# Kernel tuning notes

Hardware: AMD Instinct MI355X
Metric: run time of the kernel (lower is better)

## Reference

```python
import jax, jax.numpy as jnp
import numpy as np

N_NODES = 100000
N_EDGES = 1600000
IN_FEAT = 64
OUT_FEAT = 64


def setup_inputs() -> dict:
    key = jax.random.key(0)
    k_feat, k_src, k_dst, k_tw, k_tb, k_pw, k_pb = jax.random.split(key, 7)
    bound = 1.0 / np.sqrt(IN_FEAT)
    return {
        "feat": jax.random.normal(k_feat, (N_NODES, IN_FEAT), dtype=jnp.float32),
        "src": jax.random.randint(k_src, (N_EDGES,), 0, N_NODES, dtype=jnp.int32),
        "dst": jax.random.randint(k_dst, (N_EDGES,), 0, N_NODES, dtype=jnp.int32),
        "theta_w": jax.random.uniform(k_tw, (OUT_FEAT, IN_FEAT), jnp.float32, -bound, bound),
        "theta_b": jax.random.uniform(k_tb, (OUT_FEAT,), jnp.float32, -bound, bound),
        "phi_w": jax.random.uniform(k_pw, (OUT_FEAT, IN_FEAT), jnp.float32, -bound, bound),
        "phi_b": jax.random.uniform(k_pb, (OUT_FEAT,), jnp.float32, -bound, bound),
    }


def reference(feat, src, dst, theta_w, theta_b, phi_w, phi_b):
    # Two dense projections: h_theta = theta(feat), h_phi = phi(feat)
    h_theta = feat @ theta_w.T + theta_b          # [N, out_feat]
    h_phi = feat @ phi_w.T + phi_b                # [N, out_feat]
    diff = h_phi - h_theta                        # dstdata['x']
    # u_add_v: per-edge message e = h_theta[src] + (h_phi - h_theta)[dst]
    e = h_theta[src] + diff[dst]                  # [E, out_feat]
    # fn.max('e', 'x'): segment max over destination nodes
    out = jax.ops.segment_max(e, dst, num_segments=N_NODES)  # [N, out_feat]
    # DGL fills zero-in-degree destinations with 0 (segment_max yields -inf)
    return jnp.where(jnp.isfinite(out), out, jnp.float32(0))
```

## Files before the change

kernel.cpp:

```cpp
#include <hip/hip_runtime.h>
#include <hip/hip_bf16.h>
#include <hip/hip_fp16.h>

#define F 64
#define BSH 7
#define NBMAX 1024
#define CHUNK 4096
#define EPT 8
#define BCAP 4096
#define WPAD 72

typedef __bf16 bf16x8 __attribute__((ext_vector_type(8)));
typedef float  f32x4  __attribute__((ext_vector_type(4)));
typedef unsigned int uint4v __attribute__((ext_vector_type(4)));

__device__ inline unsigned pkmax(unsigned a, unsigned b) {
    unsigned d;
    asm volatile("v_pk_max_f16 %0, %1, %2" : "=v"(d) : "v"(a), "v"(b));
    return d;
}
__device__ inline uint4v pkmax4(uint4v a, uint4v b) {
    uint4v r;
    r.x = pkmax(a.x, b.x); r.y = pkmax(a.y, b.y);
    r.z = pkmax(a.z, b.z); r.w = pkmax(a.w, b.w);
    return r;
}
__device__ inline float half_lo(unsigned u) {
    union { unsigned short s; _Float16 h; } c; c.s = (unsigned short)(u & 0xFFFF);
    return (float)c.h;
}
__device__ inline float half_hi(unsigned u) {
    union { unsigned short s; _Float16 h; } c; c.s = (unsigned short)(u >> 16);
    return (float)c.h;
}

union FusedSh {
    struct { __bf16 w2t[128 * WPAD]; float bias[128]; } p;
    struct { int cur[NBMAX]; int gb[NBMAX]; } b;
};

__global__ __launch_bounds__(512) void fused_proj_bin(
    const float* __restrict__ feat,
    const float* __restrict__ theta_w, const float* __restrict__ theta_b,
    const float* __restrict__ phi_w,  const float* __restrict__ phi_b,
    _Float16* __restrict__ h16, _Float16* __restrict__ d16,
    const int* __restrict__ src, const int* __restrict__ dst,
    int* __restrict__ bcnt, unsigned* __restrict__ packed,
    int n_nodes, int n_edges, int nb, int bin_blocks, int proj_blocks)
{
    __shared__ FusedSh sh;
    const int t = threadIdx.x;

    if (blockIdx.x < bin_blocks) {
        const int base = blockIdx.x * CHUNK;
        const int cnt = min(CHUNK, n_edges - base);

        for (int i = t; i < nb; i += 512) sh.b.cur[i] = 0;
        __syncthreads();

        unsigned w[EPT];
        int      bk[EPT];
        int      rk[EPT];
        const int k0 = t * EPT;

        if (k0 + EPT <= cnt) {
            #pragma unroll
            for (int j = 0; j < EPT; ++j) {
                int k = k0 + j;
                int s = src[base + k], d = dst[base + k];
                w[j]  = ((unsigned)(d & ((1 << BSH) - 1)) << 17) | (unsigned)s;
                int b = d >> BSH;
                bk[j] = b;
                rk[j] = atomicAdd(&sh.b.cur[b], 1);
            }
        } else {
            #pragma unroll
            for (int j = 0; j < EPT; ++j) {
                int k = k0 + j;
                bk[j] = -1;
                if (k < cnt) {
                    int s = src[base + k], d = dst[base + k];
                    w[j]  = ((unsigned)(d & ((1 << BSH) - 1)) << 17) | (unsigned)s;
                    int b = d >> BSH;
                    bk[j] = b;
                    rk[j] = atomicAdd(&sh.b.cur[b], 1);
                }
            }
        }
        __syncthreads();

        for (int i = t; i < nb; i += 512) {
            int c = sh.b.cur[i];
            sh.b.gb[i] = c ? atomicAdd(&bcnt[i], c) : 0;
        }
        __syncthreads();

        #pragma unroll
        for (int j = 0; j < EPT; ++j) {
            if (bk[j] >= 0) {
                int pos = sh.b.gb[bk[j]] + rk[j];
                if (pos < BCAP) packed[(size_t)bk[j] * BCAP + pos] = w[j];
            }
        }
    } else {
        const int pb = blockIdx.x - bin_blocks;

        for (int i = t; i < 128 * 64; i += 512) {
            int n = i >> 6, k = i & 63;
            float v = (n < 64) ? theta_w[n * 64 + k]
                               : phi_w[(n - 64) * 64 + k] - theta_w[(n - 64) * 64 + k];
            sh.p.w2t[n * WPAD + k] = (__bf16)v;
        }
        if (t < 128) {
            int n = t;
            sh.p.bias[n] = (n < 64) ? theta_b[n] : (phi_b[n - 64] - theta_b[n - 64]);
        }
        __syncthreads();

        const int lane = t & 63;
        const int wv   = t >> 6;
        const int m    = lane & 15;
        const int q    = lane >> 4;
        const int nchunks = (n_nodes + 127) >> 7;

        for (int ch = pb; ch < nchunks; ch += proj_blocks) {
            const int rowbase = ch * 128 + wv * 16;
            int arow = rowbase + m;
            int rs = arow < n_nodes ? arow : 0;

            bf16x8 a0, a1;
            {
                const float* p0 = feat + (size_t)rs * 64 + q * 8;
                #pragma unroll
                for (int j = 0; j < 8; ++j) a0[j] = (__bf16)p0[j];
                #pragma unroll
                for (int j = 0; j < 8; ++j) a1[j] = (__bf16)p0[32 + j];
            }

            f32x4 acc[8];
            #pragma unroll
            for (int c = 0; c < 8; ++c) acc[c] = (f32x4){0.f, 0.f, 0.f, 0.f};

            #pragma unroll
            for (int c = 0; c < 8; ++c) {
                const __bf16* wp = &sh.p.w2t[(c * 16 + m) * WPAD + q * 8];
                bf16x8 b0 = *(const bf16x8*)wp;
                bf16x8 b1 = *(const bf16x8*)(wp + 32);
                acc[c] = __builtin_amdgcn_mfma_f32_16x16x32_bf16(a0, b0, acc[c], 0, 0, 0);
                acc[c] = __builtin_amdgcn_mfma_f32_16x16x32_bf16(a1, b1, acc[c], 0, 0, 0);
            }

            #pragma unroll
            for (int c = 0; c < 8; ++c) {
                float bb = sh.p.bias[c * 16 + m];
                #pragma unroll
                for (int r = 0; r < 4; ++r) {
                    int orow = rowbase + q * 4 + r;
                    if (orow < n_nodes) {
                        float v = acc[c][r] + bb;
                        if (c < 4)
                            h16[(size_t)orow * F + c * 16 + m] = (_Float16)v;
                        else
                            d16[(size_t)orow * F + (c - 4) * 16 + m] = (_Float16)v;
                    }
                }
            }
        }
    }
}

__global__ __launch_bounds__(256) void fine_kernel(
    const unsigned* __restrict__ packed, const int* __restrict__ bcnt,
    int* __restrict__ row_beg, int* __restrict__ row_end,
    int* __restrict__ sorted_src, int n_nodes)
{
    __shared__ int fcnt[128];
    __shared__ int fbeg[128];
    __shared__ int fs[256];

    const int b = blockIdx.x, t = threadIdx.x;
    const int beg = b * BCAP;
    const int cnt = min(bcnt[b], BCAP);

    if (t < 128) fcnt[t] = 0;
    __syncthreads();

    unsigned w[16];
    int      rk[16];
    #pragma unroll
    for (int j = 0; j < 16; ++j) {
        int k = j * 256 + t;
        rk[j] = -1;
        if (k < cnt) {
            unsigned wrd = packed[beg + k];
            w[j]  = wrd;
            rk[j] = atomicAdd(&fcnt[wrd >> 17], 1);
        }
    }
    __syncthreads();

    int v = (t < 128) ? fcnt[t] : 0;
    fs[t] = v;
    __syncthreads();
    for (int off = 1; off < 128; off <<= 1) {
        int x = (t >= off) ? fs[t - off] : 0;
        __syncthreads();
        fs[t] += x;
        __syncthreads();
    }
    if (t < 128) {
        int exc = fs[t] - v;
        int node = (b << BSH) + t;
        if (node < n_nodes) {
            row_beg[node] = beg + exc;
            row_end[node] = beg + exc + v;
        }
        fbeg[t] = beg + exc;
    }
    __syncthreads();

    #pragma unroll
    for (int j = 0; j < 16; ++j) {
        if (rk[j] >= 0) {
            int node = w[j] >> 17;
            sorted_src[fbeg[node] + rk[j]] = (int)(w[j] & 0x1FFFFu);
        }
    }
}

__global__ __launch_bounds__(256) void reduce_kernel(
    const int* __restrict__ row_beg, const int* __restrict__ row_end,
    const int* __restrict__ sorted_src,
    const _Float16* __restrict__ h16, const _Float16* __restrict__ d16,
    float* __restrict__ out, int n_nodes)
{
    const int wid  = (blockIdx.x * blockDim.x + threadIdx.x) >> 6;
    const int lane = threadIdx.x & 63;
    const int g    = lane >> 3;
    const int f8   = lane & 7;

    const int node = wid * 8 + g;
    const int nc   = node < n_nodes ? node : n_nodes - 1;

    const int beg = row_beg[nc];
    const int end = row_end[nc];
    const int deg = end - beg;
    const int last = beg + (deg > 0 ? deg - 1 : 0);

    int mdeg = deg;
    mdeg = max(mdeg, __shfl_xor(mdeg, 8));
    mdeg = max(mdeg, __shfl_xor(mdeg, 16));
    mdeg = max(mdeg, __shfl_xor(mdeg, 32));

    const unsigned NEG = 0xFC00FC00u;
    uint4v A = (uint4v){NEG, NEG, NEG, NEG};
    uint4v B = (uint4v){NEG, NEG, NEG, NEG};
    uint4v C = (uint4v){NEG, NEG, NEG, NEG};
    uint4v D = (uint4v){NEG, NEG, NEG, NEG};

    for (int e = 0; e < mdeg; e += 4) {
        int p0 = beg + e;     p0 = p0 < last ? p0 : last;
        int p1 = beg + e + 1; p1 = p1 < last ? p1 : last;
        int p2 = beg + e + 2; p2 = p2 < last ? p2 : last;
        int p3 = beg + e + 3; p3 = p3 < last ? p3 : last;
        int i0 = sorted_src[p0];
        int i1 = sorted_src[p1];
        int i2 = sorted_src[p2];
        int i3 = sorted_src[p3];
        uint4v v0 = *(const uint4v*)(h16 + (size_t)i0 * F + f8 * 8);
        uint4v v1 = *(const uint4v*)(h16 + (size_t)i1 * F + f8 * 8);
        uint4v v2 = *(const uint4v*)(h16 + (size_t)i2 * F + f8 * 8);
        uint4v v3 = *(const uint4v*)(h16 + (size_t)i3 * F + f8 * 8);
        A = pkmax4(A, v0);
        B = pkmax4(B, v1);
        C = pkmax4(C, v2);
        D = pkmax4(D, v3);
    }

    A = pkmax4(A, B);
    C = pkmax4(C, D);
    A = pkmax4(A, C);

    if (node < n_nodes) {
        size_t o = (size_t)node * F + f8 * 8;
        f32x4 r0, r1;
        if (deg > 0) {
            uint4v dv = __builtin_nontemporal_load((const uint4v*)(d16 + o));
            r0[0] = half_lo(dv.x) + half_lo(A.x);
            r0[1] = half_hi(dv.x) + half_hi(A.x);
            r0[2] = half_lo(dv.y) + half_lo(A.y);
            r0[3] = half_hi(dv.y) + half_hi(A.y);
            r1[0] = half_lo(dv.z) + half_lo(A.z);
            r1[1] = half_hi(dv.z) + half_hi(A.z);
            r1[2] = half_lo(dv.w) + half_lo(A.w);
            r1[3] = half_hi(dv.w) + half_hi(A.w);
        } else {
            r0 = (f32x4){0.f, 0.f, 0.f, 0.f};
            r1 = (f32x4){0.f, 0.f, 0.f, 0.f};
        }
        __builtin_nontemporal_store(r0, (f32x4*)(out + o));
        __builtin_nontemporal_store(r1, (f32x4*)(out + o + 4));
    }
}

extern "C" void kernel_launch(void* const* d_in, const int* in_sizes, int n_in,
                              void* d_out, int out_size, void* d_ws, size_t ws_size,
                              hipStream_t stream) {
    const float* feat    = (const float*)d_in[0];
    const int*   src     = (const int*)d_in[1];
    const int*   dst     = (const int*)d_in[2];
    const float* theta_w = (const float*)d_in[3];
    const float* theta_b = (const float*)d_in[4];
    const float* phi_w   = (const float*)d_in[5];
    const float* phi_b   = (const float*)d_in[6];
    float* out = (float*)d_out;

    const int n_nodes = in_sizes[0] / F;
    const int n_edges = in_sizes[1];
    const int nb      = (n_nodes + (1 << BSH) - 1) >> BSH;

    _Float16* h16        = (_Float16*)d_ws;
    _Float16* d16        = h16 + (size_t)n_nodes * F;
    unsigned* packed     = (unsigned*)(d16 + (size_t)n_nodes * F);
    int*      sorted_src = (int*)(packed + (size_t)nb * BCAP);
    int*      row_beg    = sorted_src + (size_t)nb * BCAP;
    int*      row_end    = row_beg + n_nodes;
    int*      bcnt       = row_end + n_nodes;

    hipMemsetAsync(bcnt, 0, NBMAX * sizeof(int), stream);

    const int bin_blocks  = (n_edges + CHUNK - 1) / CHUNK;
    const int proj_blocks = 391;
    fused_proj_bin<<<bin_blocks + proj_blocks, 512, 0, stream>>>(
        feat, theta_w, theta_b, phi_w, phi_b, h16, d16,
        src, dst, bcnt, packed, n_nodes, n_edges, nb, bin_blocks, proj_blocks);

    fine_kernel<<<nb, 256, 0, stream>>>(packed, bcnt, row_beg, row_end,
                                        sorted_src, n_nodes);

    int waves   = (n_nodes + 7) / 8;
    int rblocks = (waves * 64 + 255) / 256;
    reduce_kernel<<<rblocks, 256, 0, stream>>>(row_beg, row_end, sorted_src,
                                               h16, d16, out, n_nodes);
}
```

Baseline: 158.5 us.

## Fuse fine sort and reduce into one bucket kernel using LDS atomic max

Replaces the per-bucket counting sort kernel and the CSR-based gather-reduce kernel with a single kernel per 128-node bucket. Each block gathers source rows and folds them into a 128x64 shared-memory table with atomicMax on order-preserving float keys, then adds the destination term and writes out. This drops the sorted_src/row_beg/row_end round trip and one launch, at the cost of eight LDS atomics per gathered 8-element chunk, possible contention, and 32 KB of shared memory per block, which may limit occupancy.

Measured after the change: 187.9 us. 18.6% more time.

```diff
diff --git a/kernel.cpp b/kernel.cpp
--- a/kernel.cpp
+++ b/kernel.cpp
@@ -13,18 +13,8 @@
 typedef __bf16 bf16x8 __attribute__((ext_vector_type(8)));
 typedef float  f32x4  __attribute__((ext_vector_type(4)));
 typedef unsigned int uint4v __attribute__((ext_vector_type(4)));
-
-__device__ inline unsigned pkmax(unsigned a, unsigned b) {
-    unsigned d;
-    asm volatile("v_pk_max_f16 %0, %1, %2" : "=v"(d) : "v"(a), "v"(b));
-    return d;
-}
-__device__ inline uint4v pkmax4(uint4v a, uint4v b) {
-    uint4v r;
-    r.x = pkmax(a.x, b.x); r.y = pkmax(a.y, b.y);
-    r.z = pkmax(a.z, b.z); r.w = pkmax(a.w, b.w);
-    return r;
-}
+typedef unsigned int uint2v __attribute__((ext_vector_type(2)));
+
 __device__ inline float half_lo(unsigned u) {
     union { unsigned short s; _Float16 h; } c; c.s = (unsigned short)(u & 0xFFFF);
     return (float)c.h;
@@ -32,6 +22,14 @@
 __device__ inline float half_hi(unsigned u) {
     union { unsigned short s; _Float16 h; } c; c.s = (unsigned short)(u >> 16);
     return (float)c.h;
+}
+__device__ inline unsigned f32key(float x) {
+    unsigned u = __float_as_uint(x);
+    return u ^ (unsigned)(((int)u >> 31) | 0x80000000);
+}
+__device__ inline float keyf32(unsigned k) {
+    unsigned u = k ^ (unsigned)(~((int)k >> 31) | 0x80000000);
+    return __uint_as_float(u);
 }
 
 union FusedSh {
@@ -169,137 +167,62 @@
     }
 }
 
-__global__ __launch_bounds__(256) void fine_kernel(
+__global__ __launch_bounds__(256) void bucket_reduce(
     const unsigned* __restrict__ packed, const int* __restrict__ bcnt,
-    int* __restrict__ row_beg, int* __restrict__ row_end,
-    int* __restrict__ sorted_src, int n_nodes)
+    const _Float16* __restrict__ h16, const _Float16* __restrict__ d16,
+    float* __restrict__ out, int n_nodes)
 {
-    __shared__ int fcnt[128];
-    __shared__ int fbeg[128];
-    __shared__ int fs[256];
+    __shared__ unsigned mx[128 * F];
 
     const int b = blockIdx.x, t = threadIdx.x;
     const int beg = b * BCAP;
     const int cnt = min(bcnt[b], BCAP);
 
-    if (t < 128) fcnt[t] = 0;
+    #pragma unroll
+    for (int i = 0; i < 32; ++i) mx[i * 256 + t] = 0u;
     __syncthreads();
 
-    unsigned w[16];
-    int      rk[16];
-    #pragma unroll
-    for (int j = 0; j < 16; ++j) {
-        int k = j * 256 + t;
-        rk[j] = -1;
-        if (k < cnt) {
-            unsigned wrd = packed[beg + k];
-            w[j]  = wrd;
-            rk[j] = atomicAdd(&fcnt[wrd >> 17], 1);
-        }
+    const int g  = t >> 3;
+    const int f8 = t & 7;
+
+    for (int e = g; e < cnt; e += 32) {
+        unsigned wrd = packed[beg + e];
+        int srcn = (int)(wrd & 0x1FFFFu);
+        int ln   = (int)((wrd >> 17) & 127u);
+        uint4v v = *(const uint4v*)(h16 + (size_t)srcn * F + f8 * 8);
+        unsigned* base = &mx[ln * F + ((f8 * 8) ^ ((ln & 3) << 3))];
+        atomicMax(base + 0, f32key(half_lo(v.x)));
+        atomicMax(base + 1, f32key(half_hi(v.x)));
+        atomicMax(base + 2, f32key(half_lo(v.y)));
+        atomicMax(base + 3, f32key(half_hi(v.y)));
+        atomicMax(base + 4, f32key(half_lo(v.z)));
+        atomicMax(base + 5, f32key(half_hi(v.z)));
+        atomicMax(base + 6, f32key(half_lo(v.w)));
+        atomicMax(base + 7, f32key(half_hi(v.w)));
     }
     __syncthreads();
 
-    int v = (t < 128) ? fcnt[t] : 0;
-    fs[t] = v;
-    __syncthreads();
-    for (int off = 1; off < 128; off <<= 1) {
-        int x = (t >= off) ? fs[t - off] : 0;
-        __syncthreads();
-        fs[t] += x;
-        __syncthreads();
-    }
-    if (t < 128) {
-        int exc = fs[t] - v;
-        int node = (b << BSH) + t;
+    const int fb = (t & 15) * 4;
+    const int lb = t >> 4;
+    #pragma unroll
+    for (int pass = 0; pass < 8; ++pass) {
+        int ln = lb + pass * 16;
+        int node = (b << BSH) + ln;
         if (node < n_nodes) {
-            row_beg[node] = beg + exc;
-            row_end[node] = beg + exc + v;
-        }
-        fbeg[t] = beg + exc;
-    }
-    __syncthreads();
-
-    #pragma unroll
-    for (int j = 0; j < 16; ++j) {
-        if (rk[j] >= 0) {
-            int node = w[j] >> 17;
-            sorted_src[fbeg[node] + rk[j]] = (int)(w[j] & 0x1FFFFu);
-        }
-    }
-}
-
-__global__ __launch_bounds__(256) void reduce_kernel(
-    const int* __restrict__ row_beg, const int* __restrict__ row_end,
-    const int* __restrict__ sorted_src,
-    const _Float16* __restrict__ h16, const _Float16* __restrict__ d16,
-    float* __restrict__ out, int n_nodes)
-{
-    const int wid  = (blockIdx.x * blockDim.x + threadIdx.x) >> 6;
-    const int lane = threadIdx.x & 63;
-    const int g    = lane >> 3;
-    const int f8   = lane & 7;
-
-    const int node = wid * 8 + g;
-    const int nc   = node < n_nodes ? node : n_nodes - 1;
-
-    const int beg = row_beg[nc];
-    const int end = row_end[nc];
-    const int deg = end - beg;
-    const int last = beg + (deg > 0 ? deg - 1 : 0);
-
-    int mdeg = deg;
-    mdeg = max(mdeg, __shfl_xor(mdeg, 8));
-    mdeg = max(mdeg, __shfl_xor(mdeg, 16));
-    mdeg = max(mdeg, __shfl_xor(mdeg, 32));
-
-    const unsigned NEG = 0xFC00FC00u;
-    uint4v A = (uint4v){NEG, NEG, NEG, NEG};
-    uint4v B = (uint4v){NEG, NEG, NEG, NEG};
-    uint4v C = (uint4v){NEG, NEG, NEG, NEG};
-    uint4v D = (uint4v){NEG, NEG, NEG, NEG};
-
-    for (int e = 0; e < mdeg; e += 4) {
-        int p0 = beg + e;     p0 = p0 < last ? p0 : last;
-        int p1 = beg + e + 1; p1 = p1 < last ? p1 : last;
-        int p2 = beg + e + 2; p2 = p2 < last ? p2 : last;
-        int p3 = beg + e + 3; p3 = p3 < last ? p3 : last;
-        int i0 = sorted_src[p0];
-        int i1 = sorted_src[p1];
-        int i2 = sorted_src[p2];
-        int i3 = sorted_src[p3];
-        uint4v v0 = *(const uint4v*)(h16 + (size_t)i0 * F + f8 * 8);
-        uint4v v1 = *(const uint4v*)(h16 + (size_t)i1 * F + f8 * 8);
-        uint4v v2 = *(const uint4v*)(h16 + (size_t)i2 * F + f8 * 8);
-        uint4v v3 = *(const uint4v*)(h16 + (size_t)i3 * F + f8 * 8);
-        A = pkmax4(A, v0);
-        B = pkmax4(B, v1);
-        C = pkmax4(C, v2);
-        D = pkmax4(D, v3);
-    }
-
-    A = pkmax4(A, B);
-    C = pkmax4(C, D);
-    A = pkmax4(A, C);
-
-    if (node < n_nodes) {
-        size_t o = (size_t)node * F + f8 * 8;
-        f32x4 r0, r1;
-        if (deg > 0) {
-            uint4v dv = __builtin_nontemporal_load((const uint4v*)(d16 + o));
-            r0[0] = half_lo(dv.x) + half_lo(A.x);
-            r0[1] = half_hi(dv.x) + half_hi(A.x);
-            r0[2] = half_lo(dv.y) + half_lo(A.y);
-            r0[3] = half_hi(dv.y) + half_hi(A.y);
-            r1[0] = half_lo(dv.z) + half_lo(A.z);
-            r1[1] = half_hi(dv.z) + half_hi(A.z);
-            r1[2] = half_lo(dv.w) + half_lo(A.w);
-            r1[3] = half_hi(dv.w) + half_hi(A.w);
-        } else {
-            r0 = (f32x4){0.f, 0.f, 0.f, 0.f};
-            r1 = (f32x4){0.f, 0.f, 0.f, 0.f};
-        }
-        __builtin_nontemporal_store(r0, (f32x4*)(out + o));
-        __builtin_nontemporal_store(r1, (f32x4*)(out + o + 4));
+            const unsigned* kp = &mx[ln * F + (fb ^ ((ln & 3) << 3))];
+            unsigned k0 = kp[0], k1 = kp[1], k2 = kp[2], k3 = kp[3];
+            f32x4 r;
+            if (k0 != 0u) {
+                uint2v dv = *(const uint2v*)(d16 + (size_t)node * F + fb);
+                r[0] = keyf32(k0) + half_lo(dv.x);
+                r[1] = keyf32(k1) + half_hi(dv.x);
+                r[2] = keyf32(k2) + half_lo(dv.y);
+                r[3] = keyf32(k3) + half_hi(dv.y);
+            } else {
+                r = (f32x4){0.f, 0.f, 0.f, 0.f};
+            }
+            __builtin_nontemporal_store(r, (f32x4*)(out + (size_t)node * F + fb));
+        }
     }
 }
 
@@ -319,13 +242,10 @@
     const int n_edges = in_sizes[1];
     const int nb      = (n_nodes + (1 << BSH) - 1) >> BSH;
 
-    _Float16* h16        = (_Float16*)d_ws;
-    _Float16* d16        = h16 + (size_t)n_nodes * F;
-    unsigned* packed     = (unsigned*)(d16 + (size_t)n_nodes * F);
-    int*      sorted_src = (int*)(packed + (size_t)nb * BCAP);
-    int*      row_beg    = sorted_src + (size_t)nb * BCAP;
-    int*      row_end    = row_beg + n_nodes;
-    int*      bcnt       = row_end + n_nodes;
+    _Float16* h16    = (_Float16*)d_ws;
+    _Float16* d16    = h16 + (size_t)n_nodes * F;
+    unsigned* packed = (unsigned*)(d16 + (size_t)n_nodes * F);
+    int*      bcnt   = (int*)(packed + (size_t)nb * BCAP);
 
     hipMemsetAsync(bcnt, 0, NBMAX * sizeof(int), stream);
 
@@ -335,11 +255,5 @@
         feat, theta_w, theta_b, phi_w, phi_b, h16, d16,
         src, dst, bcnt, packed, n_nodes, n_edges, nb, bin_blocks, proj_blocks);
 
-    fine_kernel<<<nb, 256, 0, stream>>>(packed, bcnt, row_beg, row_end,
-                                        sorted_src, n_nodes);
-
-    int waves   = (n_nodes + 7) / 8;
-    int rblocks = (waves * 64 + 255) / 256;
-    reduce_kernel<<<rblocks, 256, 0, stream>>>(row_beg, row_end, sorted_src,
-                                               h16, d16, out, n_nodes);
-}
+    bucket_reduce<<<nb, 256, 0, stream>>>(packed, bcnt, h16, d16, out, n_nodes);
+}
```

## Fuse fine sort and segment-max reduce into one LDS-resident kernel

Applied to the files above, without the earlier changes.

Merges the per-bucket counting sort and the max reduction into a single kernel. Sorted source indices stay in shared memory instead of going to global sorted_src/row_beg/row_end. The edge list of each 128-node bucket is then split evenly across 32 thread groups, and per-node partial maxima are combined in LDS with CAS-based packed-half max. This removes one kernel launch and a global round trip, and balances work across uneven degrees. In exchange it adds CAS loops, a binary search per group, larger LDS use that may lower occupancy, and only nb (~782) blocks of 256 threads.

Measured after the change: 151.5 us. 1.05x faster.

```diff
diff --git a/kernel.cpp b/kernel.cpp
--- a/kernel.cpp
+++ b/kernel.cpp
@@ -32,6 +32,16 @@
 __device__ inline float half_hi(unsigned u) {
     union { unsigned short s; _Float16 h; } c; c.s = (unsigned short)(u >> 16);
     return (float)c.h;
+}
+__device__ inline void casmax(unsigned* a, unsigned val) {
+    unsigned old = *a;
+    while (true) {
+        unsigned nw = pkmax(old, val);
+        if (nw == old) break;
+        unsigned prev = atomicCAS(a, old, nw);
+        if (prev == old) break;
+        old = prev;
+    }
 }
 
 union FusedSh {
@@ -169,19 +179,24 @@
     }
 }
 
-__global__ __launch_bounds__(256) void fine_kernel(
+__global__ __launch_bounds__(256) void sort_reduce(
     const unsigned* __restrict__ packed, const int* __restrict__ bcnt,
-    int* __restrict__ row_beg, int* __restrict__ row_end,
-    int* __restrict__ sorted_src, int n_nodes)
+    const _Float16* __restrict__ h16, const _Float16* __restrict__ d16,
+    float* __restrict__ out, int n_nodes)
 {
+    __shared__ unsigned ew[BCAP];
+    __shared__ unsigned mx[128 * 32];
     __shared__ int fcnt[128];
-    __shared__ int fbeg[128];
+    __shared__ int fbg[129];
     __shared__ int fs[256];
 
     const int b = blockIdx.x, t = threadIdx.x;
     const int beg = b * BCAP;
     const int cnt = min(bcnt[b], BCAP);
-
+    const unsigned NEGI = 0xFC00FC00u;
+
+    #pragma unroll
+    for (int i = 0; i < 16; ++i) mx[i * 256 + t] = NEGI;
     if (t < 128) fcnt[t] = 0;
     __syncthreads();
 
@@ -208,98 +223,122 @@
         fs[t] += x;
         __syncthreads();
     }
-    if (t < 128) {
-        int exc = fs[t] - v;
-        int node = (b << BSH) + t;
-        if (node < n_nodes) {
-            row_beg[node] = beg + exc;
-            row_end[node] = beg + exc + v;
-        }
-        fbeg[t] = beg + exc;
-    }
+    if (t < 128) fbg[t] = fs[t] - v;
+    if (t == 0)  fbg[128] = cnt;
     __syncthreads();
 
     #pragma unroll
     for (int j = 0; j < 16; ++j) {
         if (rk[j] >= 0) {
-            int node = w[j] >> 17;
-            sorted_src[fbeg[node] + rk[j]] = (int)(w[j] & 0x1FFFFu);
-        }
-    }
-}
-
-__global__ __launch_bounds__(256) void reduce_kernel(
-    const int* __restrict__ row_beg, const int* __restrict__ row_end,
-    const int* __restrict__ sorted_src,
-    const _Float16* __restrict__ h16, const _Float16* __restrict__ d16,
-    float* __restrict__ out, int n_nodes)
-{
-    const int wid  = (blockIdx.x * blockDim.x + threadIdx.x) >> 6;
-    const int lane = threadIdx.x & 63;
-    const int g    = lane >> 3;
-    const int f8   = lane & 7;
-
-    const int node = wid * 8 + g;
-    const int nc   = node < n_nodes ? node : n_nodes - 1;
-
-    const int beg = row_beg[nc];
-    const int end = row_end[nc];
-    const int deg = end - beg;
-    const int last = beg + (deg > 0 ? deg - 1 : 0);
-
-    int mdeg = deg;
-    mdeg = max(mdeg, __shfl_xor(mdeg, 8));
-    mdeg = max(mdeg, __shfl_xor(mdeg, 16));
-    mdeg = max(mdeg, __shfl_xor(mdeg, 32));
-
-    const unsigned NEG = 0xFC00FC00u;
-    uint4v A = (uint4v){NEG, NEG, NEG, NEG};
-    uint4v B = (uint4v){NEG, NEG, NEG, NEG};
-    uint4v C = (uint4v){NEG, NEG, NEG, NEG};
-    uint4v D = (uint4v){NEG, NEG, NEG, NEG};
-
-    for (int e = 0; e < mdeg; e += 4) {
-        int p0 = beg + e;     p0 = p0 < last ? p0 : last;
-        int p1 = beg + e + 1; p1 = p1 < last ? p1 : last;
-        int p2 = beg + e + 2; p2 = p2 < last ? p2 : last;
-        int p3 = beg + e + 3; p3 = p3 < last ? p3 : last;
-        int i0 = sorted_src[p0];
-        int i1 = sorted_src[p1];
-        int i2 = sorted_src[p2];
-        int i3 = sorted_src[p3];
-        uint4v v0 = *(const uint4v*)(h16 + (size_t)i0 * F + f8 * 8);
-        uint4v v1 = *(const uint4v*)(h16 + (size_t)i1 * F + f8 * 8);
-        uint4v v2 = *(const uint4v*)(h16 + (size_t)i2 * F + f8 * 8);
-        uint4v v3 = *(const uint4v*)(h16 + (size_t)i3 * F + f8 * 8);
-        A = pkmax4(A, v0);
-        B = pkmax4(B, v1);
-        C = pkmax4(C, v2);
-        D = pkmax4(D, v3);
-    }
-
-    A = pkmax4(A, B);
-    C = pkmax4(C, D);
-    A = pkmax4(A, C);
-
-    if (node < n_nodes) {
-        size_t o = (size_t)node * F + f8 * 8;
-        f32x4 r0, r1;
-        if (deg > 0) {
-            uint4v dv = __builtin_nontemporal_load((const uint4v*)(d16 + o));
-            r0[0] = half_lo(dv.x) + half_lo(A.x);
-            r0[1] = half_hi(dv.x) + half_hi(A.x);
-            r0[2] = half_lo(dv.y) + half_lo(A.y);
-            r0[3] = half_hi(dv.y) + half_hi(A.y);
-            r1[0] = half_lo(dv.z) + half_lo(A.z);
-            r1[1] = half_hi(dv.z) + half_hi(A.z);
-            r1[2] = half_lo(dv.w) + half_lo(A.w);
-            r1[3] = half_hi(dv.w) + half_hi(A.w);
-        } else {
-            r0 = (f32x4){0.f, 0.f, 0.f, 0.f};
-            r1 = (f32x4){0.f, 0.f, 0.f, 0.f};
-        }
-        __builtin_nontemporal_store(r0, (f32x4*)(out + o));
-        __builtin_nontemporal_store(r1, (f32x4*)(out + o + 4));
+            unsigned wrd = w[j];
+            ew[fbg[wrd >> 17] + rk[j]] = wrd & 0x1FFFFu;
+        }
+    }
+    __syncthreads();
+
+    const int g  = t >> 3;
+    const int f8 = t & 7;
+    {
+        int L0 = (cnt + 31) >> 5;
+        int L  = ((L0 + 3) & ~7) | 4;
+        int s  = g * L; if (s > cnt) s = cnt;
+        int e  = s + L; if (e > cnt) e = cnt;
+
+        if (s < e) {
+            int lo = 0, hi = 128;
+            while (lo + 1 < hi) {
+                int mid = (lo + hi) >> 1;
+                if (fbg[mid] <= s) lo = mid; else hi = mid;
+            }
+            int node = lo;
+            int nend = fbg[node + 1];
+
+            uint4v acc = (uint4v){NEGI, NEGI, NEGI, NEGI};
+            int p = s;
+            for (; p + 4 <= e; p += 4) {
+                uint4v sv = *(const uint4v*)&ew[p];
+                uint4v v0 = *(const uint4v*)(h16 + (size_t)sv.x * F + f8 * 8);
+                uint4v v1 = *(const uint4v*)(h16 + (size_t)sv.y * F + f8 * 8);
+                uint4v v2 = *(const uint4v*)(h16 + (size_t)sv.z * F + f8 * 8);
+                uint4v v3 = *(const uint4v*)(h16 + (size_t)sv.w * F + f8 * 8);
+                while (p >= nend) {
+                    unsigned* m0 = &mx[node * 32 + f8 * 4];
+                    casmax(m0 + 0, acc.x); casmax(m0 + 1, acc.y);
+                    casmax(m0 + 2, acc.z); casmax(m0 + 3, acc.w);
+                    acc = (uint4v){NEGI, NEGI, NEGI, NEGI};
+                    ++node; nend = fbg[node + 1];
+                }
+                acc = pkmax4(acc, v0);
+                while (p + 1 >= nend) {
+                    unsigned* m0 = &mx[node * 32 + f8 * 4];
+                    casmax(m0 + 0, acc.x); casmax(m0 + 1, acc.y);
+                    casmax(m0 + 2, acc.z); casmax(m0 + 3, acc.w);
+                    acc = (uint4v){NEGI, NEGI, NEGI, NEGI};
+                    ++node; nend = fbg[node + 1];
+                }
+                acc = pkmax4(acc, v1);
+                while (p + 2 >= nend) {
+                    unsigned* m0 = &mx[node * 32 + f8 * 4];
+                    casmax(m0 + 0, acc.x); casmax(m0 + 1, acc.y);
+                    casmax(m0 + 2, acc.z); casmax(m0 + 3, acc.w);
+                    acc = (uint4v){NEGI, NEGI, NEGI, NEGI};
+                    ++node; nend = fbg[node + 1];
+                }
+                acc = pkmax4(acc, v2);
+                while (p + 3 >= nend) {
+                    unsigned* m0 = &mx[node * 32 + f8 * 4];
+                    casmax(m0 + 0, acc.x); casmax(m0 + 1, acc.y);
+                    casmax(m0 + 2, acc.z); casmax(m0 + 3, acc.w);
+                    acc = (uint4v){NEGI, NEGI, NEGI, NEGI};
+                    ++node; nend = fbg[node + 1];
+                }
+                acc = pkmax4(acc, v3);
+            }
+            for (; p < e; ++p) {
+                unsigned srcn = ew[p];
+                uint4v v0 = *(const uint4v*)(h16 + (size_t)srcn * F + f8 * 8);
+                while (p >= nend) {
+                    unsigned* m0 = &mx[node * 32 + f8 * 4];
+                    casmax(m0 + 0, acc.x); casmax(m0 + 1, acc.y);
+                    casmax(m0 + 2, acc.z); casmax(m0 + 3, acc.w);
+                    acc = (uint4v){NEGI, NEGI, NEGI, NEGI};
+                    ++node; nend = fbg[node + 1];
+                }
+                acc = pkmax4(acc, v0);
+            }
+            unsigned* m0 = &mx[node * 32 + f8 * 4];
+            casmax(m0 + 0, acc.x); casmax(m0 + 1, acc.y);
+            casmax(m0 + 2, acc.z); casmax(m0 + 3, acc.w);
+        }
+    }
+    __syncthreads();
+
+    const int ln0 = t >> 3;
+    #pragma unroll
+    for (int pass = 0; pass < 4; ++pass) {
+        int ln = ln0 + pass * 32;
+        int node = (b << BSH) + ln;
+        if (node < n_nodes) {
+            size_t o = (size_t)node * F + f8 * 8;
+            f32x4 r0, r1;
+            if (fcnt[ln] > 0) {
+                uint4v A  = *(const uint4v*)&mx[ln * 32 + f8 * 4];
+                uint4v dv = __builtin_nontemporal_load((const uint4v*)(d16 + o));
+                r0[0] = half_lo(dv.x) + half_lo(A.x);
+                r0[1] = half_hi(dv.x) + half_hi(A.x);
+                r0[2] = half_lo(dv.y) + half_lo(A.y);
+                r0[3] = half_hi(dv.y) + half_hi(A.y);
+                r1[0] = half_lo(dv.z) + half_lo(A.z);
+                r1[1] = half_hi(dv.z) + half_hi(A.z);
+                r1[2] = half_lo(dv.w) + half_lo(A.w);
+                r1[3] = half_hi(dv.w) + half_hi(A.w);
+            } else {
+                r0 = (f32x4){0.f, 0.f, 0.f, 0.f};
+                r1 = (f32x4){0.f, 0.f, 0.f, 0.f};
+            }
+            __builtin_nontemporal_store(r0, (f32x4*)(out + o));
+            __builtin_nontemporal_store(r1, (f32x4*)(out + o + 4));
+        }
     }
 }
 
@@ -319,13 +358,10 @@
     const int n_edges = in_sizes[1];
     const int nb      = (n_nodes + (1 << BSH) - 1) >> BSH;
 
-    _Float16* h16        = (_Float16*)d_ws;
-    _Float16* d16        = h16 + (size_t)n_nodes * F;
-    unsigned* packed     = (unsigned*)(d16 + (size_t)n_nodes * F);
-    int*      sorted_src = (int*)(packed + (size_t)nb * BCAP);
-    int*      row_beg    = sorted_src + (size_t)nb * BCAP;
-    int*      row_end    = row_beg + n_nodes;
-    int*      bcnt       = row_end + n_nodes;
+    _Float16* h16    = (_Float16*)d_ws;
+    _Float16* d16    = h16 + (size_t)n_nodes * F;
+    unsigned* packed = (unsigned*)(d16 + (size_t)n_nodes * F);
+    int*      bcnt   = (int*)(packed + (size_t)nb * BCAP);
 
     hipMemsetAsync(bcnt, 0, NBMAX * sizeof(int), stream);
 
@@ -335,11 +371,5 @@
         feat, theta_w, theta_b, phi_w, phi_b, h16, d16,
         src, dst, bcnt, packed, n_nodes, n_edges, nb, bin_blocks, proj_blocks);
 
-    fine_kernel<<<nb, 256, 0, stream>>>(packed, bcnt, row_beg, row_end,
-                                        sorted_src, n_nodes);
-
-    int waves   = (n_nodes + 7) / 8;
-    int rblocks = (waves * 64 + 255) / 256;
-    reduce_kernel<<<rblocks, 256, 0, stream>>>(row_beg, row_end, sorted_src,
-                                               h16, d16, out, n_nodes);
-}
+    sort_reduce<<<nb, 256, 0, stream>>>(packed, bcnt, h16, d16, out, n_nodes);
+}
```
